# Kernel optimization log

Measured on AMD Instinct MI355X. Metric: run time of the kernel, lower is better.

The kernel has to match this reference:

```python
import jax, jax.numpy as jnp
from jax import lax
import numpy as np

N_TAGS = 16      # number of pos-tag experts
N_PRI = 4        # first N_PRI tags are privacy terms
UNK_ID = 0
VOCAB = 40000    # parser word vocabulary
M = 1024         # per-tag target vocab size
E = 100          # parser embedding dim
WED = 200        # word embedding dim (input encoder)
PED = 56         # pos embedding dim (input encoder)
H = 512          # ctx_fs (per-direction LSTM hidden)
TEMP = 1.0       # eval-mode gumbel temperature
ENT_PEN = 0.01


def _lstm(x, mask, Wx, Wh, b, reverse):
    # x: [B, L, D], mask: [B, L]; returns hidden states [B, L, H]
    B = x.shape[0]
    Hd = Wh.shape[0]
    gates_x = jnp.einsum('bld,dg->blg', x, Wx) + b  # precompute input part of gates

    def step(carry, inp):
        h, c = carry
        gx, m = inp  # gx: [B, 4H], m: [B, 1]
        gates = gx + h @ Wh
        i, f, g, o = jnp.split(gates, 4, axis=-1)
        i = jax.nn.sigmoid(i)
        f = jax.nn.sigmoid(f)
        g = jnp.tanh(g)
        o = jax.nn.sigmoid(o)
        c_new = f * c + i * g
        h_new = o * jnp.tanh(c_new)
        # masked update (padded steps keep previous state)
        h_new = h_new * m + h * (1.0 - m)
        c_new = c_new * m + c * (1.0 - m)
        return (h_new, c_new), h_new

    seq = (jnp.swapaxes(gates_x, 0, 1), jnp.swapaxes(mask, 0, 1)[..., None])
    init = (jnp.zeros((B, Hd), x.dtype), jnp.zeros((B, Hd), x.dtype))
    _, hs = lax.scan(step, init, seq, reverse=reverse)
    return jnp.swapaxes(hs, 0, 1)


def setup_inputs():
    key = jax.random.key(0)
    ks = jax.random.split(key, 16)
    B, L = 32, 256
    D = WED + PED  # 256
    inp = {}
    inp['inp_word'] = jax.random.randint(ks[0], (B, L), 0, VOCAB, dtype=jnp.int32)
    inp['inp_pos'] = jax.random.randint(ks[1], (B, L), 0, N_TAGS, dtype=jnp.int32)
    inp['inp_mask'] = jnp.ones((B, L), jnp.float32)
    inp['gumbel_u'] = jax.random.uniform(ks[2], (B * L, M), jnp.float32)
    inp['word_emb'] = jax.random.normal(ks[3], (VOCAB, WED), jnp.float32) * 0.1
    inp['pos_emb'] = jax.random.normal(ks[4], (N_TAGS, PED), jnp.float32) * 0.1
    inp['Wx_f'] = jax.random.normal(ks[5], (D, 4 * H), jnp.float32) * 0.05
    inp['Wh_f'] = jax.random.normal(ks[6], (H, 4 * H), jnp.float32) * 0.05
    inp['b_f'] = jnp.zeros((4 * H,), jnp.float32)
    inp['Wx_b'] = jax.random.normal(ks[7], (D, 4 * H), jnp.float32) * 0.05
    inp['Wh_b'] = jax.random.normal(ks[8], (H, 4 * H), jnp.float32) * 0.05
    inp['b_b'] = jnp.zeros((4 * H,), jnp.float32)
    inp['dec_W'] = jax.random.normal(ks[9], (N_TAGS, 2 * H, M), jnp.float32) * 0.03
    inp['dec_b'] = jnp.zeros((N_TAGS, M), jnp.float32)
    inp['words_tbl'] = jax.random.randint(ks[10], (N_TAGS, M), 0, VOCAB, dtype=jnp.int32)
    inp['psr_weight'] = jax.random.normal(ks[11], (VOCAB, E), jnp.float32) * 0.1
    return inp


def reference(inp_word, inp_pos, inp_mask, gumbel_u, word_emb, pos_emb,
              Wx_f, Wh_f, b_f, Wx_b, Wh_b, b_b, dec_W, dec_b, words_tbl, psr_weight):
    B, L = inp_word.shape
    # input encoder: word + pos embedding concat
    x = jnp.concatenate([word_emb[inp_word], pos_emb[inp_pos]], axis=-1)
    # bidirectional masked LSTM context
    hf = _lstm(x, inp_mask, Wx_f, Wh_f, b_f, reverse=False)
    hb = _lstm(x, inp_mask, Wx_b, Wh_b, b_b, reverse=True)
    ctx = jnp.concatenate([hf, hb], axis=-1).reshape(B * L, 2 * H)

    pos = inp_pos.reshape(-1)            # [T]
    wflat = inp_word.reshape(-1)         # [T]
    g = -jnp.log(-jnp.log(gumbel_u + 1e-10) + 1e-10)  # gumbel noise [T, M]

    obf_word = wflat
    obf_emb = psr_weight[wflat]          # [T, E]
    entropy = jnp.float32(0.0)
    for p in range(N_TAGS):  # loop over fixed small expert set
        m = pos == p                                    # routing mask [T]
        logp = jax.nn.log_softmax(ctx @ dec_W[p] + dec_b[p], axis=-1)  # [T, M]
        n = jnp.sum(m).astype(logp.dtype)
        ent_p = jnp.sum((-logp * jnp.exp(logp)) * m[:, None]) / jnp.maximum(n * M, 1.0)
        entropy = entropy + jnp.where(n > 0, ent_p, 0.0)
        spt = jax.nn.softmax((logp + g) / TEMP, axis=-1)  # gumbel-softmax sample
        widx = words_tbl[p][jnp.argmax(spt, axis=-1)]
        obf_word = jnp.where(m, widx, obf_word)
        emb = spt @ psr_weight[words_tbl[p]]              # [T, E]
        obf_emb = jnp.where(m[:, None], emb, obf_emb)

    obf_mask = pos < N_TAGS   # all tags are target tags
    pri_mask = pos < N_PRI
    avoid = (obf_word == wflat) & obf_mask
    obf_word = jnp.where(avoid, UNK_ID, obf_word)
    obf_emb = jnp.where(avoid[:, None], psr_weight[UNK_ID], obf_emb)
    ent_loss = -entropy * ENT_PEN
    return (obf_word.reshape(B, L), obf_emb.reshape(B, L, E),
            obf_mask.reshape(B, L), pri_mask.reshape(B, L), ent_loss)
```

## Files before the change

kernel.cpp:

```cpp
#include <hip/hip_runtime.h>
#include <math.h>
#include <cstdint>

#define BB 32
#define LL 256
#define TT 8192
#define DIN 256
#define WEDm 200
#define PEDm 56
#define HH 512
#define G4 2048
#define MM 1024
#define EE 100
#define NTAGS 16

__global__ void k_embed(const int* __restrict__ word, const int* __restrict__ posi,
                        const float* __restrict__ wemb, const float* __restrict__ pemb,
                        float* __restrict__ X) {
  int t = blockIdx.x;
  int c = threadIdx.x * 4;
  float4 v;
  if (c < WEDm) {
    int w = word[t];
    v = *(const float4*)(wemb + (size_t)w * WEDm + c);
  } else {
    int p = posi[t];
    v = *(const float4*)(pemb + (size_t)p * PEDm + (c - WEDm));
  }
  *(float4*)(X + (size_t)t * DIN + c) = v;
}

__global__ __launch_bounds__(256) void k_gemm_bias(const float* __restrict__ A,
    const float* __restrict__ W, const float* __restrict__ bias,
    float* __restrict__ C, int Mm, int Nn, int Kk) {
  __shared__ float As[16][68];
  __shared__ float Bs[16][64];
  int tid = threadIdx.x;
  int tx = tid & 15, ty = tid >> 4;
  int row0 = blockIdx.y * 64, col0 = blockIdx.x * 64;
  float acc[4][4] = {};
  for (int k0 = 0; k0 < Kk; k0 += 16) {
    int r = tid >> 2, c = (tid & 3) * 4;
    float4 av = *(const float4*)(A + (size_t)(row0 + r) * Kk + k0 + c);
    As[c + 0][r] = av.x; As[c + 1][r] = av.y; As[c + 2][r] = av.z; As[c + 3][r] = av.w;
    int r2 = tid >> 4, c2 = (tid & 15) * 4;
    float4 bv = *(const float4*)(W + (size_t)(k0 + r2) * Nn + col0 + c2);
    *(float4*)(&Bs[r2][c2]) = bv;
    __syncthreads();
#pragma unroll
    for (int kk = 0; kk < 16; ++kk) {
      float4 a4 = *(const float4*)(&As[kk][ty * 4]);
      float4 b4 = *(const float4*)(&Bs[kk][tx * 4]);
      float a[4] = {a4.x, a4.y, a4.z, a4.w};
      float b[4] = {b4.x, b4.y, b4.z, b4.w};
#pragma unroll
      for (int i = 0; i < 4; ++i)
#pragma unroll
        for (int j = 0; j < 4; ++j)
          acc[i][j] += a[i] * b[j];
    }
    __syncthreads();
  }
#pragma unroll
  for (int i = 0; i < 4; ++i) {
    int row = row0 + ty * 4 + i;
#pragma unroll
    for (int j = 0; j < 4; ++j) {
      int col = col0 + tx * 4 + j;
      C[(size_t)row * Nn + col] = acc[i][j] + bias[col];
    }
  }
}

template <int N>
__device__ __forceinline__ float ror_add(float x) {
  int xi = __float_as_int(x);
  int yi = __builtin_amdgcn_update_dpp(xi, xi, 0x100 + N, 0xF, 0xF, false);
  return x + __int_as_float(yi);
}

__device__ __forceinline__ float sigm(float x) { return 1.f / (1.f + __expf(-x)); }

__global__ __launch_bounds__(512, 1) void k_lstm5(
    const float* __restrict__ Whf, const float* __restrict__ Whb,
    const float* __restrict__ GXfp, const float* __restrict__ GXbp,
    const float* __restrict__ maskp, float* __restrict__ Hbuf,
    float* __restrict__ ctx, int* __restrict__ flags) {
  extern __shared__ float lds[];
  float* Whs  = lds;
  float* Hs   = lds;
  float* part = lds + 16512;
  const int tid = threadIdx.x;
  const int wg  = blockIdx.x;
  const int dir = wg & 1;
  const int grp = wg >> 1;
  const int j0  = grp * 4;
  const float* Wh = dir ? Whb : Whf;
  const float* GX = dir ? GXbp : GXfp;

  const int ks = tid & 31;
  const int cq = (tid >> 5) & 3;
  const int bq = tid >> 7;
  const int uu = tid & 3, bb = tid >> 2;

  for (int i = tid; i < 16 * 512; i += 512) {
    int c = i >> 9, k = i & 511;
    Whs[c * 512 + k] = Wh[(size_t)k * G4 + (c >> 2) * HH + j0 + (c & 3)];
  }
  __syncthreads();
  float4 wreg[4][4];
#pragma unroll
  for (int ci = 0; ci < 4; ++ci)
#pragma unroll
    for (int j = 0; j < 4; ++j)
      wreg[ci][j] = *(const float4*)(Whs + (cq * 4 + ci) * 512 + 4 * ks + 128 * j);
  __syncthreads();

  if (tid < 128) {
    __hip_atomic_store(&Hbuf[(size_t)(0 * 2 + dir) * 16384 + bb * HH + j0 + uu], 0.f,
                       __ATOMIC_RELAXED, __HIP_MEMORY_SCOPE_AGENT);
  }
  asm volatile("s_waitcnt vmcnt(0)" ::: "memory");
  __syncthreads();
  if (tid == 0)
    __hip_atomic_store(&flags[wg], 1, __ATOMIC_RELAXED, __HIP_MEMORY_SCOPE_AGENT);

  float cstate = 0.f;
  int par = 0;

  for (int s = 0; s < LL; ++s) {
    const int t = dir ? (LL - 1 - s) : s;

    float gx0 = 0.f, gx1 = 0.f, gx2 = 0.f, gx3 = 0.f, mval = 0.f;
    if (tid < 128) {
      const float* gp = GX + ((size_t)(bb * LL + t)) * G4 + j0 + uu;
      gx0 = gp[0]; gx1 = gp[512]; gx2 = gp[1024]; gx3 = gp[1536];
      mval = maskp[bb * LL + t];
    }

    if (tid < 128) {
      int it = 0;
      while (__hip_atomic_load(&flags[2 * tid + dir], __ATOMIC_RELAXED,
                               __HIP_MEMORY_SCOPE_AGENT) < s + 1) {
        __builtin_amdgcn_s_sleep(1);
        if (++it > (1 << 20)) break;
      }
    }
    __syncthreads();
    __builtin_amdgcn_sched_barrier(0);

    {
      const unsigned long long* hb64 =
          (const unsigned long long*)(Hbuf + (size_t)(par * 2 + dir) * 16384);
      unsigned long long hv[16];
#pragma unroll
      for (int m = 0; m < 16; ++m)
        hv[m] = __hip_atomic_load(&hb64[tid + 512 * m], __ATOMIC_RELAXED,
                                  __HIP_MEMORY_SCOPE_AGENT);
#pragma unroll
      for (int m = 0; m < 16; ++m) {
        int f = 2 * (tid + 512 * m);
        int b = f >> 9, k = f & 511;
        *(float2*)(&Hs[b * 516 + k]) = *(float2*)(&hv[m]);
      }
    }
    __syncthreads();

    float acc[4][8];
#pragma unroll
    for (int ci = 0; ci < 4; ++ci)
#pragma unroll
      for (int bi = 0; bi < 8; ++bi) acc[ci][bi] = 0.f;
    {
      const float* hp = Hs + (bq * 8) * 516 + 4 * ks;
#pragma unroll
      for (int j = 0; j < 4; ++j) {
        const int ko = 128 * j;
        float4 h4[8];
#pragma unroll
        for (int bi = 0; bi < 8; ++bi) h4[bi] = *(const float4*)(hp + bi * 516 + ko);
#pragma unroll
        for (int ci = 0; ci < 4; ++ci) {
          float4 w = wreg[ci][j];
#pragma unroll
          for (int bi = 0; bi < 8; ++bi) {
            float4 h = h4[bi];
            acc[ci][bi] += w.x * h.x + w.y * h.y + w.z * h.z + w.w * h.w;
          }
        }
      }
    }
#pragma unroll
    for (int ci = 0; ci < 4; ++ci)
#pragma unroll
      for (int bi = 0; bi < 8; ++bi) {
        float v = acc[ci][bi];
        v = ror_add<1>(v); v = ror_add<2>(v); v = ror_add<4>(v); v = ror_add<8>(v);
        acc[ci][bi] = v;
      }
    if ((ks & 15) == 0) {
      const int ph = ks >> 4;
      float* dst = part + ph * 576 + (cq * 4) * 36 + bq * 8;
#pragma unroll
      for (int ci = 0; ci < 4; ++ci) {
        *(float4*)(dst + ci * 36 + 0) = make_float4(acc[ci][0], acc[ci][1], acc[ci][2], acc[ci][3]);
        *(float4*)(dst + ci * 36 + 4) = make_float4(acc[ci][4], acc[ci][5], acc[ci][6], acc[ci][7]);
      }
    }
    __syncthreads();

    float hn = 0.f;
    if (tid < 128) {
      float pre[4];
#pragma unroll
      for (int q = 0; q < 4; ++q) {
        int c = q * 4 + uu;
        pre[q] = part[c * 36 + bb] + part[576 + c * 36 + bb];
      }
      pre[0] += gx0; pre[1] += gx1; pre[2] += gx2; pre[3] += gx3;
      float gi = sigm(pre[0]);
      float gf = sigm(pre[1]);
      float gg = tanhf(pre[2]);
      float go = sigm(pre[3]);
      float cnew = gf * cstate + gi * gg;
      float hnew = go * tanhf(cnew);
      float hold = Hs[bb * 516 + j0 + uu];
      hn = hnew * mval + hold * (1.f - mval);
      cstate = cnew * mval + cstate * (1.f - mval);
      __hip_atomic_store(&Hbuf[(size_t)((par ^ 1) * 2 + dir) * 16384 + bb * HH + j0 + uu],
                         hn, __ATOMIC_RELAXED, __HIP_MEMORY_SCOPE_AGENT);
    }
    asm volatile("s_waitcnt vmcnt(0)" ::: "memory");
    __syncthreads();
    if (tid == 0)
      __hip_atomic_store(&flags[wg], s + 2, __ATOMIC_RELAXED, __HIP_MEMORY_SCOPE_AGENT);
    if (tid < 128)
      ctx[((size_t)(bb * LL + t)) * (2 * HH) + dir * HH + j0 + uu] = hn;
    par ^= 1;
  }
}

__global__ void k_init0(int* __restrict__ flags) { flags[threadIdx.x] = 0; }

__global__ void k_zero16(int* counts) { if (threadIdx.x < 16) counts[threadIdx.x] = 0; }

__global__ void k_count(const int* __restrict__ posi, int* __restrict__ counts) {
  int t = blockIdx.x * 256 + threadIdx.x;
  if (t < TT) atomicAdd(&counts[posi[t]], 1);
}

__global__ void k_prefix(const int* __restrict__ counts, int* __restrict__ offs) {
  if (threadIdx.x == 0) {
    int a = 0;
    for (int p = 0; p < NTAGS; ++p) { offs[p] = a; a += counts[p]; }
    offs[NTAGS] = a;
  }
}

__global__ __launch_bounds__(256) void k_compact(const int* __restrict__ posi,
    const int* __restrict__ offs, int* __restrict__ idxlist) {
  int p = blockIdx.x, tid = threadIdx.x;
  __shared__ int sc[256];
  __shared__ int sbase;
  if (tid == 0) sbase = offs[p];
  __syncthreads();
  for (int c0 = 0; c0 < TT; c0 += 256) {
    int t = c0 + tid;
    int f = (posi[t] == p) ? 1 : 0;
    int v = f;
    sc[tid] = v;
    __syncthreads();
    for (int o = 1; o < 256; o <<= 1) {
      int add = (tid >= o) ? sc[tid - o] : 0;
      __syncthreads();
      v += add;
      sc[tid] = v;
      __syncthreads();
    }
    int total = sc[255];
    int base = sbase;
    if (f) idxlist[base + v - 1] = t;
    __syncthreads();
    if (tid == 0) sbase = base + total;
    __syncthreads();
  }
}

__global__ void k_ptbl(const int* __restrict__ wtbl, const float* __restrict__ psrw,
                       float* __restrict__ Ptbl) {
  int i = blockIdx.x * 256 + threadIdx.x;
  int total = NTAGS * MM * EE;
  for (; i < total; i += gridDim.x * 256) {
    int p = i / (MM * EE);
    int rem = i - p * (MM * EE);
    int r = rem / EE;
    int e = rem - r * EE;
    Ptbl[i] = psrw[(size_t)wtbl[p * MM + r] * EE + e];
  }
}

__global__ __launch_bounds__(256) void k_decgemm(const float* __restrict__ ctxb,
    const float* __restrict__ decW, const float* __restrict__ decb,
    const int* __restrict__ counts, const int* __restrict__ offs,
    const int* __restrict__ idxlist, float* __restrict__ Z) {
  int p = blockIdx.z;
  int n = counts[p];
  int r0 = blockIdx.y * 64;
  if (r0 >= n) return;
  int col0 = blockIdx.x * 64;
  __shared__ float As[16][68];
  __shared__ float Bs[16][64];
  __shared__ int rows[64];
  int tid = threadIdx.x;
  if (tid < 64) {
    int r = r0 + tid;
    rows[tid] = idxlist[offs[p] + (r < n ? r : 0)];
  }
  __syncthreads();
  const float* W = decW + (size_t)p * MM * MM;
  float acc[4][4] = {};
  for (int k0 = 0; k0 < MM; k0 += 16) {
    int r = tid >> 2, c = (tid & 3) * 4;
    float4 av = *(const float4*)(ctxb + (size_t)rows[r] * MM + k0 + c);
    As[c + 0][r] = av.x; As[c + 1][r] = av.y; As[c + 2][r] = av.z; As[c + 3][r] = av.w;
    int r2 = tid >> 4, c2 = (tid & 15) * 4;
    float4 bv = *(const float4*)(W + (size_t)(k0 + r2) * MM + col0 + c2);
    *(float4*)(&Bs[r2][c2]) = bv;
    __syncthreads();
#pragma unroll
    for (int kk = 0; kk < 16; ++kk) {
      float4 a4 = *(const float4*)(&As[kk][(tid >> 4) * 4]);
      float4 b4 = *(const float4*)(&Bs[kk][(tid & 15) * 4]);
      float a[4] = {a4.x, a4.y, a4.z, a4.w};
      float b[4] = {b4.x, b4.y, b4.z, b4.w};
#pragma unroll
      for (int i = 0; i < 4; ++i)
#pragma unroll
        for (int j = 0; j < 4; ++j)
          acc[i][j] += a[i] * b[j];
    }
    __syncthreads();
  }
  int tx = tid & 15, ty = tid >> 4;
#pragma unroll
  for (int i = 0; i < 4; ++i) {
    int r = r0 + ty * 4 + i;
    if (r < n) {
      int tok = rows[ty * 4 + i];
#pragma unroll
      for (int j = 0; j < 4; ++j) {
        int col = col0 + tx * 4 + j;
        Z[(size_t)tok * MM + col] = acc[i][j] + decb[p * MM + col];
      }
    }
  }
}

__global__ __launch_bounds__(256) void k_softmax(
    const float* __restrict__ Z, const float* __restrict__ gum,
    const int* __restrict__ posi, const int* __restrict__ wflat,
    const int* __restrict__ wtbl, float* __restrict__ SPT,
    float* __restrict__ rowent, int* __restrict__ avoidb,
    float* __restrict__ out_word, float* __restrict__ out_mask,
    float* __restrict__ out_pri) {
  __shared__ float red[256];
  __shared__ float redv[256];
  __shared__ int redi[256];
  int t = blockIdx.x, tid = threadIdx.x;
  float z[4];
#pragma unroll
  for (int i = 0; i < 4; ++i) z[i] = Z[(size_t)t * MM + tid + 256 * i];
  float mx = fmaxf(fmaxf(z[0], z[1]), fmaxf(z[2], z[3]));
  red[tid] = mx; __syncthreads();
  for (int o = 128; o > 0; o >>= 1) { if (tid < o) red[tid] = fmaxf(red[tid], red[tid + o]); __syncthreads(); }
  mx = red[0]; __syncthreads();
  float se = 0.f;
#pragma unroll
  for (int i = 0; i < 4; ++i) se += expf(z[i] - mx);
  red[tid] = se; __syncthreads();
  for (int o = 128; o > 0; o >>= 1) { if (tid < o) red[tid] += red[tid + o]; __syncthreads(); }
  float lse = logf(red[0]); __syncthreads();
  float lp[4]; float ent = 0.f;
#pragma unroll
  for (int i = 0; i < 4; ++i) { lp[i] = z[i] - mx - lse; ent -= lp[i] * expf(lp[i]); }
  red[tid] = ent; __syncthreads();
  for (int o = 128; o > 0; o >>= 1) { if (tid < o) red[tid] += red[tid + o]; __syncthreads(); }
  float enttot = red[0]; __syncthreads();
  float y[4];
#pragma unroll
  for (int i = 0; i < 4; ++i) {
    float u = gum[(size_t)t * MM + tid + 256 * i];
    float g = -logf(-logf(u + 1e-10f) + 1e-10f);
    y[i] = lp[i] + g;
  }
  float bv = y[0]; int bi = tid;
#pragma unroll
  for (int i = 1; i < 4; ++i) { int j = tid + 256 * i; if (y[i] > bv) { bv = y[i]; bi = j; } }
  redv[tid] = bv; redi[tid] = bi; __syncthreads();
  for (int o = 128; o > 0; o >>= 1) {
    if (tid < o) {
      float v2 = redv[tid + o]; int i2 = redi[tid + o];
      if (v2 > redv[tid] || (v2 == redv[tid] && i2 < redi[tid])) { redv[tid] = v2; redi[tid] = i2; }
    }
    __syncthreads();
  }
  float ymax = redv[0]; int amax = redi[0]; __syncthreads();
  float e[4]; float s2 = 0.f;
#pragma unroll
  for (int i = 0; i < 4; ++i) { e[i] = expf(y[i] - ymax); s2 += e[i]; }
  red[tid] = s2; __syncthreads();
  for (int o = 128; o > 0; o >>= 1) { if (tid < o) red[tid] += red[tid + o]; __syncthreads(); }
  float inv = 1.f / red[0];
#pragma unroll
  for (int i = 0; i < 4; ++i) SPT[(size_t)t * MM + tid + 256 * i] = e[i] * inv;
  if (tid == 0) {
    int p = posi[t];
    int widx = wtbl[p * MM + amax];
    int wf = wflat[t];
    int avoid = (widx == wf) ? 1 : 0;
    avoidb[t] = avoid;
    out_word[t] = (float)(avoid ? 0 : widx);
    out_mask[t] = 1.0f;
    out_pri[t] = (p < 4) ? 1.0f : 0.0f;
    rowent[t] = enttot;
  }
}

__global__ __launch_bounds__(256) void k_embgemm(const float* __restrict__ SPT,
    const float* __restrict__ Ptbl, const float* __restrict__ psrw,
    const int* __restrict__ counts, const int* __restrict__ offs,
    const int* __restrict__ idxlist, const int* __restrict__ avoidb,
    float* __restrict__ out_emb) {
  int p = blockIdx.y;
  int n = counts[p];
  int r0 = blockIdx.x * 64;
  if (r0 >= n) return;
  __shared__ float As[16][68];
  __shared__ float Bs[16][132];
  __shared__ int rows[64];
  int tid = threadIdx.x;
  if (tid < 64) rows[tid] = idxlist[offs[p] + ((r0 + tid) < n ? (r0 + tid) : 0)];
  __syncthreads();
  const float* P = Ptbl + (size_t)p * MM * EE;
  int tx = tid & 31, ty = tid >> 5;
  float acc[8][4] = {};
  for (int k0 = 0; k0 < MM; k0 += 16) {
    int r = tid >> 2, c = (tid & 3) * 4;
    float4 av = *(const float4*)(SPT + (size_t)rows[r] * MM + k0 + c);
    As[c + 0][r] = av.x; As[c + 1][r] = av.y; As[c + 2][r] = av.z; As[c + 3][r] = av.w;
    int r2 = tid >> 4;
    int c2 = (tid & 15) * 8;
    float4 b0 = make_float4(0.f, 0.f, 0.f, 0.f), b1 = make_float4(0.f, 0.f, 0.f, 0.f);
    if (c2 + 3 < EE) b0 = *(const float4*)(P + (size_t)(k0 + r2) * EE + c2);
    if (c2 + 7 < EE) b1 = *(const float4*)(P + (size_t)(k0 + r2) * EE + c2 + 4);
    *(float4*)(&Bs[r2][c2]) = b0;
    *(float4*)(&Bs[r2][c2 + 4]) = b1;
    __syncthreads();
#pragma unroll
    for (int kk = 0; kk < 16; ++kk) {
      float4 b4 = *(const float4*)(&Bs[kk][tx * 4]);
      float4 a0 = *(const float4*)(&As[kk][ty * 8]);
      float4 a1 = *(const float4*)(&As[kk][ty * 8 + 4]);
      float a[8] = {a0.x, a0.y, a0.z, a0.w, a1.x, a1.y, a1.z, a1.w};
#pragma unroll
      for (int ri = 0; ri < 8; ++ri) {
        acc[ri][0] += a[ri] * b4.x; acc[ri][1] += a[ri] * b4.y;
        acc[ri][2] += a[ri] * b4.z; acc[ri][3] += a[ri] * b4.w;
      }
    }
    __syncthreads();
  }
#pragma unroll
  for (int ri = 0; ri < 8; ++ri) {
    int r = ty * 8 + ri;
    if (r0 + r < n) {
      int tok = rows[r];
      int av = avoidb[tok];
#pragma unroll
      for (int j = 0; j < 4; ++j) {
        int col = tx * 4 + j;
        if (col < EE) {
          float v = av ? psrw[col] : acc[ri][j];
          out_emb[(size_t)tok * EE + col] = v;
        }
      }
    }
  }
}

__global__ __launch_bounds__(256) void k_final(const float* __restrict__ rowent,
    const int* __restrict__ posi, const int* __restrict__ counts,
    float* __restrict__ out_loss) {
  __shared__ float red[256];
  int tid = threadIdx.x;
  float s = 0.f;
  for (int t = tid; t < TT; t += 256) {
    int p = posi[t];
    float denom = fmaxf((float)counts[p] * (float)MM, 1.0f);
    s += rowent[t] / denom;
  }
  red[tid] = s; __syncthreads();
  for (int o = 128; o > 0; o >>= 1) { if (tid < o) red[tid] += red[tid + o]; __syncthreads(); }
  if (tid == 0) out_loss[0] = -red[0] * 0.01f;
}

extern "C" void kernel_launch(void* const* d_in, const int* in_sizes, int n_in,
                              void* d_out, int out_size, void* d_ws, size_t ws_size,
                              hipStream_t stream) {
  const int*   inp_word = (const int*)d_in[0];
  const int*   inp_pos  = (const int*)d_in[1];
  const float* inp_mask = (const float*)d_in[2];
  const float* gum      = (const float*)d_in[3];
  const float* wemb     = (const float*)d_in[4];
  const float* pemb     = (const float*)d_in[5];
  const float* Wx_f     = (const float*)d_in[6];
  const float* Wh_f     = (const float*)d_in[7];
  const float* b_f      = (const float*)d_in[8];
  const float* Wx_b     = (const float*)d_in[9];
  const float* Wh_b     = (const float*)d_in[10];
  const float* b_b      = (const float*)d_in[11];
  const float* decW     = (const float*)d_in[12];
  const float* decb     = (const float*)d_in[13];
  const int*   wtbl     = (const int*)d_in[14];
  const float* psrw     = (const float*)d_in[15];

  float* out_word = (float*)d_out;
  float* out_emb  = out_word + TT;
  float* out_mask = out_emb + (size_t)TT * EE;
  float* out_pri  = out_mask + TT;
  float* out_loss = out_pri + TT;

  float* ws = (float*)d_ws;
  float* X      = ws;
  float* GXf    = X + (size_t)TT * DIN;
  float* GXb    = GXf + (size_t)TT * G4;
  float* ctxb   = GXb + (size_t)TT * G4;
  float* Hbuf   = ctxb + (size_t)TT * MM;
  float* rowent = Hbuf + 2 * 2 * BB * HH;
  int* avoidb   = (int*)(rowent + TT);
  int* counts   = avoidb + TT;
  int* offs     = counts + 16;
  int* idxlist  = offs + 32;
  int* flags    = idxlist + TT;
  float* Z    = GXf;
  float* SPT  = Z;
  float* Ptbl = GXb;

  k_embed<<<TT, 64, 0, stream>>>(inp_word, inp_pos, wemb, pemb, X);
  k_gemm_bias<<<dim3(G4 / 64, TT / 64), 256, 0, stream>>>(X, Wx_f, b_f, GXf, TT, G4, DIN);
  k_gemm_bias<<<dim3(G4 / 64, TT / 64), 256, 0, stream>>>(X, Wx_b, b_b, GXb, TT, G4, DIN);

  k_init0<<<1, 256, 0, stream>>>(flags);
  {
    const int ldsz = (16512 + 1152) * 4;
    hipFuncSetAttribute((const void*)k_lstm5,
                        hipFuncAttributeMaxDynamicSharedMemorySize, ldsz);
    k_lstm5<<<256, 512, ldsz, stream>>>(Wh_f, Wh_b, GXf, GXb, inp_mask, Hbuf, ctxb, flags);
  }

  k_zero16<<<1, 64, 0, stream>>>(counts);
  k_count<<<TT / 256, 256, 0, stream>>>(inp_pos, counts);
  k_prefix<<<1, 64, 0, stream>>>(counts, offs);
  k_compact<<<NTAGS, 256, 0, stream>>>(inp_pos, offs, idxlist);
  k_ptbl<<<1024, 256, 0, stream>>>(wtbl, psrw, Ptbl);
  k_decgemm<<<dim3(MM / 64, TT / 64, NTAGS), 256, 0, stream>>>(ctxb, decW, decb, counts, offs, idxlist, Z);
  k_softmax<<<TT, 256, 0, stream>>>(Z, gum, inp_pos, inp_word, wtbl, SPT, rowent, avoidb,
                                    out_word, out_mask, out_pri);
  k_embgemm<<<dim3(TT / 64, NTAGS), 256, 0, stream>>>(SPT, Ptbl, psrw, counts, offs, idxlist,
                                                      avoidb, out_emb);
  k_final<<<1, 256, 0, stream>>>(rowent, inp_pos, counts, out_loss);
}
```

Measured before the change: 2.549 ms.

## Repartition persistent LSTM blocks over batch groups and hidden units

```diff
diff --git a/kernel.cpp b/kernel.cpp
--- a/kernel.cpp
+++ b/kernel.cpp
@@ -81,44 +81,51 @@
 
 __device__ __forceinline__ float sigm(float x) { return 1.f / (1.f + __expf(-x)); }
 
-__global__ __launch_bounds__(512, 1) void k_lstm5(
+__global__ __launch_bounds__(512, 1) void k_lstm6(
     const float* __restrict__ Whf, const float* __restrict__ Whb,
     const float* __restrict__ GXfp, const float* __restrict__ GXbp,
     const float* __restrict__ maskp, float* __restrict__ Hbuf,
     float* __restrict__ ctx, int* __restrict__ flags) {
   extern __shared__ float lds[];
-  float* Whs  = lds;
+  float* Wtmp = lds;
   float* Hs   = lds;
-  float* part = lds + 16512;
+  float* part = lds + 8 * 516;
   const int tid = threadIdx.x;
   const int wg  = blockIdx.x;
   const int dir = wg & 1;
-  const int grp = wg >> 1;
-  const int j0  = grp * 4;
+  const int bg  = (wg >> 1) & 3;
+  const int ug  = wg >> 3;
+  const int j0  = ug * 16;
+  const int b0  = bg * 8;
   const float* Wh = dir ? Whb : Whf;
   const float* GX = dir ? GXbp : GXfp;
 
   const int ks = tid & 31;
-  const int cq = (tid >> 5) & 3;
-  const int bq = tid >> 7;
-  const int uu = tid & 3, bb = tid >> 2;
-
-  for (int i = tid; i < 16 * 512; i += 512) {
-    int c = i >> 9, k = i & 511;
-    Whs[c * 512 + k] = Wh[(size_t)k * G4 + (c >> 2) * HH + j0 + (c & 3)];
-  }
-  __syncthreads();
+  const int cq = tid >> 5;
+  const int uu = tid & 15, bloc = tid >> 4;
+
   float4 wreg[4][4];
 #pragma unroll
-  for (int ci = 0; ci < 4; ++ci)
-#pragma unroll
-    for (int j = 0; j < 4; ++j)
-      wreg[ci][j] = *(const float4*)(Whs + (cq * 4 + ci) * 512 + 4 * ks + 128 * j);
-  __syncthreads();
+  for (int cc = 0; cc < 4; ++cc) {
+    for (int i = tid; i < 16 * 512; i += 512) {
+      int c = i >> 9, k = i & 511;
+      Wtmp[c * 512 + k] = Wh[(size_t)k * G4 + cc * HH + j0 + c];
+    }
+    __syncthreads();
+    if ((cq >> 2) == cc) {
+      int cbase = (cq & 3) * 4;
+#pragma unroll
+      for (int ci = 0; ci < 4; ++ci)
+#pragma unroll
+        for (int j = 0; j < 4; ++j)
+          wreg[ci][j] = *(const float4*)(Wtmp + (cbase + ci) * 512 + 4 * ks + 128 * j);
+    }
+    __syncthreads();
+  }
 
   if (tid < 128) {
-    __hip_atomic_store(&Hbuf[(size_t)(0 * 2 + dir) * 16384 + bb * HH + j0 + uu], 0.f,
-                       __ATOMIC_RELAXED, __HIP_MEMORY_SCOPE_AGENT);
+    __hip_atomic_store(&Hbuf[(size_t)(0 * 2 + dir) * 16384 + (b0 + bloc) * HH + j0 + uu],
+                       0.f, __ATOMIC_RELAXED, __HIP_MEMORY_SCOPE_AGENT);
   }
   asm volatile("s_waitcnt vmcnt(0)" ::: "memory");
   __syncthreads();
@@ -133,14 +140,14 @@
 
     float gx0 = 0.f, gx1 = 0.f, gx2 = 0.f, gx3 = 0.f, mval = 0.f;
     if (tid < 128) {
-      const float* gp = GX + ((size_t)(bb * LL + t)) * G4 + j0 + uu;
+      const float* gp = GX + ((size_t)((b0 + bloc) * LL + t)) * G4 + j0 + uu;
       gx0 = gp[0]; gx1 = gp[512]; gx2 = gp[1024]; gx3 = gp[1536];
-      mval = maskp[bb * LL + t];
-    }
-
-    if (tid < 128) {
+      mval = maskp[(b0 + bloc) * LL + t];
+    }
+
+    if (tid < 32) {
       int it = 0;
-      while (__hip_atomic_load(&flags[2 * tid + dir], __ATOMIC_RELAXED,
+      while (__hip_atomic_load(&flags[(tid * 4 + bg) * 2 + dir], __ATOMIC_RELAXED,
                                __HIP_MEMORY_SCOPE_AGENT) < s + 1) {
         __builtin_amdgcn_s_sleep(1);
         if (++it > (1 << 20)) break;
@@ -151,14 +158,14 @@
 
     {
       const unsigned long long* hb64 =
-          (const unsigned long long*)(Hbuf + (size_t)(par * 2 + dir) * 16384);
-      unsigned long long hv[16];
-#pragma unroll
-      for (int m = 0; m < 16; ++m)
+          (const unsigned long long*)(Hbuf + (size_t)(par * 2 + dir) * 16384 + b0 * HH);
+      unsigned long long hv[4];
+#pragma unroll
+      for (int m = 0; m < 4; ++m)
         hv[m] = __hip_atomic_load(&hb64[tid + 512 * m], __ATOMIC_RELAXED,
                                   __HIP_MEMORY_SCOPE_AGENT);
 #pragma unroll
-      for (int m = 0; m < 16; ++m) {
+      for (int m = 0; m < 4; ++m) {
         int f = 2 * (tid + 512 * m);
         int b = f >> 9, k = f & 511;
         *(float2*)(&Hs[b * 516 + k]) = *(float2*)(&hv[m]);
@@ -172,7 +179,7 @@
 #pragma unroll
       for (int bi = 0; bi < 8; ++bi) acc[ci][bi] = 0.f;
     {
-      const float* hp = Hs + (bq * 8) * 516 + 4 * ks;
+      const float* hp = Hs + 4 * ks;
 #pragma unroll
       for (int j = 0; j < 4; ++j) {
         const int ko = 128 * j;
@@ -200,11 +207,11 @@
       }
     if ((ks & 15) == 0) {
       const int ph = ks >> 4;
-      float* dst = part + ph * 576 + (cq * 4) * 36 + bq * 8;
+      float* dst = part + ph * 768 + (cq * 4) * 12;
 #pragma unroll
       for (int ci = 0; ci < 4; ++ci) {
-        *(float4*)(dst + ci * 36 + 0) = make_float4(acc[ci][0], acc[ci][1], acc[ci][2], acc[ci][3]);
-        *(float4*)(dst + ci * 36 + 4) = make_float4(acc[ci][4], acc[ci][5], acc[ci][6], acc[ci][7]);
+        *(float4*)(dst + ci * 12 + 0) = make_float4(acc[ci][0], acc[ci][1], acc[ci][2], acc[ci][3]);
+        *(float4*)(dst + ci * 12 + 4) = make_float4(acc[ci][4], acc[ci][5], acc[ci][6], acc[ci][7]);
       }
     }
     __syncthreads();
@@ -214,8 +221,8 @@
       float pre[4];
 #pragma unroll
       for (int q = 0; q < 4; ++q) {
-        int c = q * 4 + uu;
-        pre[q] = part[c * 36 + bb] + part[576 + c * 36 + bb];
+        int lc = q * 16 + uu;
+        pre[q] = part[lc * 12 + bloc] + part[768 + lc * 12 + bloc];
       }
       pre[0] += gx0; pre[1] += gx1; pre[2] += gx2; pre[3] += gx3;
       float gi = sigm(pre[0]);
@@ -224,10 +231,10 @@
       float go = sigm(pre[3]);
       float cnew = gf * cstate + gi * gg;
       float hnew = go * tanhf(cnew);
-      float hold = Hs[bb * 516 + j0 + uu];
+      float hold = Hs[bloc * 516 + j0 + uu];
       hn = hnew * mval + hold * (1.f - mval);
       cstate = cnew * mval + cstate * (1.f - mval);
-      __hip_atomic_store(&Hbuf[(size_t)((par ^ 1) * 2 + dir) * 16384 + bb * HH + j0 + uu],
+      __hip_atomic_store(&Hbuf[(size_t)((par ^ 1) * 2 + dir) * 16384 + (b0 + bloc) * HH + j0 + uu],
                          hn, __ATOMIC_RELAXED, __HIP_MEMORY_SCOPE_AGENT);
     }
     asm volatile("s_waitcnt vmcnt(0)" ::: "memory");
@@ -235,7 +242,7 @@
     if (tid == 0)
       __hip_atomic_store(&flags[wg], s + 2, __ATOMIC_RELAXED, __HIP_MEMORY_SCOPE_AGENT);
     if (tid < 128)
-      ctx[((size_t)(bb * LL + t)) * (2 * HH) + dir * HH + j0 + uu] = hn;
+      ctx[((size_t)((b0 + bloc) * LL + t)) * (2 * HH) + dir * HH + j0 + uu] = hn;
     par ^= 1;
   }
 }
@@ -552,10 +559,10 @@
 
   k_init0<<<1, 256, 0, stream>>>(flags);
   {
-    const int ldsz = (16512 + 1152) * 4;
-    hipFuncSetAttribute((const void*)k_lstm5,
+    const int ldsz = 32768;
+    hipFuncSetAttribute((const void*)k_lstm6,
                         hipFuncAttributeMaxDynamicSharedMemorySize, ldsz);
-    k_lstm5<<<256, 512, ldsz, stream>>>(Wh_f, Wh_b, GXf, GXb, inp_mask, Hbuf, ctxb, flags);
+    k_lstm6<<<256, 512, ldsz, stream>>>(Wh_f, Wh_b, GXf, GXb, inp_mask, Hbuf, ctxb, flags);
   }
 
   k_zero16<<<1, 64, 0, stream>>>(counts);
```

Result: faster. 2.330 ms (-8.6%).
